# Optimization experiments

Measured on AMD Instinct MI355X. Metric: run time of the kernel, lower is better.

## Reference

```python
import jax, jax.numpy as jnp
import numpy as np

SEQ, BATCH, IN, HID, OUT = 512, 4096, 9, 64, 10


def setup_inputs() -> dict:
    key = jax.random.key(0)
    ks = jax.random.split(key, 11)
    s = 1.0 / np.sqrt(HID)
    u = lambda k, shp: jax.random.uniform(k, shp, jnp.float32, -s, s)
    return {
        "x": jax.random.normal(ks[0], (SEQ, BATCH, IN), jnp.float32),
        "W_ih0": u(ks[1], (HID, IN)),
        "W_hh0": u(ks[2], (HID, HID)),
        "b_ih0": u(ks[3], (HID,)),
        "b_hh0": u(ks[4], (HID,)),
        "W_ih1": u(ks[5], (HID, HID)),
        "W_hh1": u(ks[6], (HID, HID)),
        "b_ih1": u(ks[7], (HID,)),
        "b_hh1": u(ks[8], (HID,)),
        "W_fc": u(ks[9], (OUT, HID)),
        "b_fc": u(ks[10], (OUT,)),
    }


def _rnn_layer(x, W_ih, W_hh, b_ih, b_hh):
    # x: (seq, batch, d_in) -> (seq, batch, hid); h_t = tanh(x_t W_ih^T + b_ih + h_{t-1} W_hh^T + b_hh)
    xw = jnp.einsum('sbi,hi->sbh', x, W_ih) + (b_ih + b_hh)  # precompute input proj
    h0 = jnp.zeros((x.shape[1], W_hh.shape[0]), x.dtype)

    def step(h, xw_t):
        h = jnp.tanh(xw_t + h @ W_hh.T)
        return h, h

    _, out = jax.lax.scan(step, h0, xw)
    return out


def reference(x, W_ih0, W_hh0, b_ih0, b_hh0, W_ih1, W_hh1, b_ih1, b_hh1, W_fc, b_fc):
    h1 = _rnn_layer(x, W_ih0, W_hh0, b_ih0, b_hh0)   # (seq, batch, hid)
    h2 = _rnn_layer(h1, W_ih1, W_hh1, b_ih1, b_hh1)  # (seq, batch, hid)
    # Faithful to original quirk: rnn_out[:, -1, :] on a (seq, batch, hid) tensor
    # selects the last BATCH element for every timestep -> (seq, hid)
    feat = h2[:, -1, :]
    return feat @ W_fc.T + b_fc  # (seq, out)
```

## Files before the change

### kernel.cpp

```cpp
#include <hip/hip_runtime.h>

#define SEQn   512
#define BATCHn 4096
#define INn    9
#define HIDn   64
#define OUTn   10

typedef __attribute__((ext_vector_type(4))) float f32x4;
typedef _Float16 half2_t __attribute__((ext_vector_type(2)));
typedef unsigned short u16;
typedef unsigned int   u32;

#if __has_builtin(__builtin_amdgcn_fdot2)
#define DOT2(a,b,c) __builtin_amdgcn_fdot2((a),(b),(c),false)
#else
__device__ __forceinline__ float DOT2(half2_t a, half2_t b, float c){
    return __builtin_fmaf((float)a.x,(float)b.x, __builtin_fmaf((float)a.y,(float)b.y,c));
}
#endif
#define H2(u) __builtin_bit_cast(half2_t, (u))

__device__ __forceinline__ float fast_tanh(float x){
    float e = __builtin_amdgcn_exp2f(x * 2.8853900817779268f);
    float r = __builtin_amdgcn_rcpf(e + 1.0f);
    return __builtin_fmaf(-2.0f, r, 1.0f);
}
__device__ __forceinline__ u16 f2h(float v){
    return __builtin_bit_cast(u16, (_Float16)v);
}

__device__ __forceinline__ void load_w16(const float* __restrict__ W, int row, half2_t* wr){
#pragma unroll
    for (int c = 0; c < 16; ++c){
        f32x4 v = *(const f32x4*)&W[row*HIDn + c*4];
        wr[2*c]   = half2_t{(_Float16)v.x, (_Float16)v.y};
        wr[2*c+1] = half2_t{(_Float16)v.z, (_Float16)v.w};
    }
}

__device__ __forceinline__ float dot64r(const uint4* v, const half2_t* wr, float acc){
    float a0 = acc, a1 = 0.f, a2 = 0.f, a3 = 0.f;
#pragma unroll
    for (int jb = 0; jb < 8; ++jb){
        a0 = DOT2(H2(v[jb].x), wr[jb*4+0], a0);
        a1 = DOT2(H2(v[jb].y), wr[jb*4+1], a1);
        a2 = DOT2(H2(v[jb].z), wr[jb*4+2], a2);
        a3 = DOT2(H2(v[jb].w), wr[jb*4+3], a3);
    }
    return (a0 + a1) + (a2 + a3);
}

extern "C" __global__ __launch_bounds__(256, 1)
void rnn_lastrow(const float* __restrict__ x,
                 const float* __restrict__ Wih0, const float* __restrict__ Whh0,
                 const float* __restrict__ bih0, const float* __restrict__ bhh0,
                 const float* __restrict__ Wih1, const float* __restrict__ Whh1,
                 const float* __restrict__ bih1, const float* __restrict__ bhh1,
                 const float* __restrict__ Wfc,  const float* __restrict__ bfc,
                 float* __restrict__ out)
{
    __shared__ __align__(16) u16   xl16[SEQn*16];
    __shared__ __align__(16) float u2r[64*HIDn];
    __shared__ __align__(16) u16   h1buf[HIDn];
    __shared__ __align__(16) u16   h2buf[HIDn];
    __shared__ u32 wm[2];

    const int tid  = threadIdx.x;
    const int w    = tid >> 6;
    const int lane = tid & 63;
    volatile u32* vwm = wm;

    for (int idx = tid; idx < SEQn*16; idx += 256){
        int t = idx >> 4, j = idx & 15;
        float v = (j < INn) ? x[((long)t*BATCHn + (BATCHn-1))*INn + j] : 0.f;
        xl16[idx] = f2h(v);
    }
    if (tid < 64){ h1buf[tid] = 0; h2buf[tid] = 0; }
    if (tid == 0){ wm[0] = 0u; wm[1] = 0u; }
    __syncthreads();
    if (w >= 2) return;

    if (w == 0){
        half2_t wr0[32], wr1[32], wx[5];
        load_w16(Whh0, lane, wr0);
        load_w16(Wih1, lane, wr1);
        const float* wxr = Wih0 + lane*INn;
#pragma unroll
        for (int p = 0; p < 4; ++p)
            wx[p] = half2_t{(_Float16)wxr[2*p], (_Float16)wxr[2*p+1]};
        wx[4] = half2_t{(_Float16)wxr[8], (_Float16)0.f};
        const float b1 = bih0[lane] + bhh0[lane];
        const float b2 = bih1[lane] + bhh1[lane];

        uint4 va[8], vb[8];

        auto w0step = [&](int p, uint4* CUR, const uint4* PRV){
            if ((p & 7) == 0){
                asm volatile("s_waitcnt lgkmcnt(0)" ::: "memory");
                vwm[0] = (p >= 2) ? (u32)(p - 2) : 0u;
                while (vwm[1] + 58u <= (u32)p) __builtin_amdgcn_s_sleep(2);
            }
#pragma unroll
            for (int j = 0; j < 8; ++j) CUR[j] = ((const uint4*)h1buf)[j];
            const u32* xr = (const u32*)(xl16 + p*16);
            uint4 xa = *(const uint4*)xr;
            u32  xb = xr[4];
            if (p >= 2){
                float u2v = dot64r(PRV, wr1, b2);
                u2r[((p-2)&63)*HIDn + lane] = u2v;
            }
            float u1 = b1;
            u1 = DOT2(H2(xa.x), wx[0], u1);
            u1 = DOT2(H2(xa.y), wx[1], u1);
            u1 = DOT2(H2(xa.z), wx[2], u1);
            u1 = DOT2(H2(xa.w), wx[3], u1);
            u1 = DOT2(H2(xb),   wx[4], u1);
            float y = dot64r(CUR, wr0, 0.f);
            h1buf[lane] = f2h(fast_tanh(y + u1));
        };

        for (int p = 0; p < SEQn; p += 2){
            w0step(p,     va, vb);
            w0step(p + 1, vb, va);
        }
        {
            float u2v = dot64r(vb, wr1, b2);
            u2r[(510 & 63)*HIDn + lane] = u2v;
            uint4 vf[8];
#pragma unroll
            for (int j = 0; j < 8; ++j) vf[j] = ((const uint4*)h1buf)[j];
            u2v = dot64r(vf, wr1, b2);
            u2r[(511 & 63)*HIDn + lane] = u2v;
            asm volatile("s_waitcnt lgkmcnt(0)" ::: "memory");
            vwm[0] = (u32)SEQn;
        }
    } else {
        half2_t wr2[32], wfc[32];
        load_w16(Whh1, lane, wr2);
        load_w16(Wfc, (lane < OUTn) ? lane : (OUTn-1), wfc);
        const float bo = (lane < OUTn) ? bfc[lane] : 0.f;

        uint4 va[8], vb[8];

        auto w1step = [&](int c, uint4* CUR, const uint4* PRV){
            if ((c & 7) == 0){
                vwm[1] = (u32)c;
                while (vwm[0] < (u32)(c + 8)) __builtin_amdgcn_s_sleep(2);
            }
#pragma unroll
            for (int j = 0; j < 8; ++j) CUR[j] = ((const uint4*)h2buf)[j];
            float u2v = *((volatile float*)&u2r[(c & 63)*HIDn + lane]);
            if (c >= 2 && lane < OUTn){
                float fc = dot64r(PRV, wfc, bo);
                out[(c-2)*OUTn + lane] = fc;
            }
            float y = dot64r(CUR, wr2, u2v);
            h2buf[lane] = f2h(fast_tanh(y));
        };

        for (int c = 0; c < SEQn; c += 2){
            w1step(c,     va, vb);
            w1step(c + 1, vb, va);
        }
        if (lane < OUTn){
            float fc = dot64r(vb, wfc, bo);
            out[510*OUTn + lane] = fc;
        }
        {
            uint4 vf[8];
#pragma unroll
            for (int j = 0; j < 8; ++j) vf[j] = ((const uint4*)h2buf)[j];
            if (lane < OUTn){
                float fc = dot64r(vf, wfc, bo);
                out[511*OUTn + lane] = fc;
            }
        }
    }
}

extern "C" void kernel_launch(void* const* d_in, const int* in_sizes, int n_in,
                              void* d_out, int out_size, void* d_ws, size_t ws_size,
                              hipStream_t stream){
    rnn_lastrow<<<dim3(1), dim3(256), 0, stream>>>(
        (const float*)d_in[0],
        (const float*)d_in[1], (const float*)d_in[2],
        (const float*)d_in[3], (const float*)d_in[4],
        (const float*)d_in[5], (const float*)d_in[6],
        (const float*)d_in[7], (const float*)d_in[8],
        (const float*)d_in[9], (const float*)d_in[10],
        (float*)d_out);
}
```

Before: 270.8 us.

## Replace per-lane fdot2 recurrence with MFMA 16x16x16 matvecs kept in registers

Result: slower. 394.2 us (+45.6%).

```diff
diff --git a/kernel.cpp b/kernel.cpp
--- a/kernel.cpp
+++ b/kernel.cpp
@@ -6,48 +6,22 @@
 #define HIDn   64
 #define OUTn   10
 
-typedef __attribute__((ext_vector_type(4))) float f32x4;
-typedef _Float16 half2_t __attribute__((ext_vector_type(2)));
+typedef __attribute__((ext_vector_type(4))) float    f32x4;
+typedef __attribute__((ext_vector_type(4))) _Float16 f16x4;
 typedef unsigned short u16;
 typedef unsigned int   u32;
 
-#if __has_builtin(__builtin_amdgcn_fdot2)
-#define DOT2(a,b,c) __builtin_amdgcn_fdot2((a),(b),(c),false)
-#else
-__device__ __forceinline__ float DOT2(half2_t a, half2_t b, float c){
-    return __builtin_fmaf((float)a.x,(float)b.x, __builtin_fmaf((float)a.y,(float)b.y,c));
-}
-#endif
-#define H2(u) __builtin_bit_cast(half2_t, (u))
-
-__device__ __forceinline__ float fast_tanh(float x){
-    float e = __builtin_amdgcn_exp2f(x * 2.8853900817779268f);
+#define MFMA16(A,B,C) __builtin_amdgcn_mfma_f32_16x16x16f16((A),(B),(C),0,0,0)
+
+__device__ __forceinline__ float tanh_pre(float x){
+    float e = __builtin_amdgcn_exp2f(x);
     float r = __builtin_amdgcn_rcpf(e + 1.0f);
     return __builtin_fmaf(-2.0f, r, 1.0f);
 }
-__device__ __forceinline__ u16 f2h(float v){
-    return __builtin_bit_cast(u16, (_Float16)v);
-}
-
-__device__ __forceinline__ void load_w16(const float* __restrict__ W, int row, half2_t* wr){
-#pragma unroll
-    for (int c = 0; c < 16; ++c){
-        f32x4 v = *(const f32x4*)&W[row*HIDn + c*4];
-        wr[2*c]   = half2_t{(_Float16)v.x, (_Float16)v.y};
-        wr[2*c+1] = half2_t{(_Float16)v.z, (_Float16)v.w};
-    }
-}
-
-__device__ __forceinline__ float dot64r(const uint4* v, const half2_t* wr, float acc){
-    float a0 = acc, a1 = 0.f, a2 = 0.f, a3 = 0.f;
-#pragma unroll
-    for (int jb = 0; jb < 8; ++jb){
-        a0 = DOT2(H2(v[jb].x), wr[jb*4+0], a0);
-        a1 = DOT2(H2(v[jb].y), wr[jb*4+1], a1);
-        a2 = DOT2(H2(v[jb].z), wr[jb*4+2], a2);
-        a3 = DOT2(H2(v[jb].w), wr[jb*4+3], a3);
-    }
-    return (a0 + a1) + (a2 + a3);
+__device__ __forceinline__ u16 f2h(float v){ return __builtin_bit_cast(u16, (_Float16)v); }
+__device__ __forceinline__ f16x4 cvt4(f32x4 a){
+    f16x4 r = {(_Float16)a.x, (_Float16)a.y, (_Float16)a.z, (_Float16)a.w};
+    return r;
 }
 
 extern "C" __global__ __launch_bounds__(256, 1)
@@ -61,119 +35,196 @@
 {
     __shared__ __align__(16) u16   xl16[SEQn*16];
     __shared__ __align__(16) float u2r[64*HIDn];
-    __shared__ __align__(16) u16   h1buf[HIDn];
-    __shared__ __align__(16) u16   h2buf[HIDn];
     __shared__ u32 wm[2];
 
     const int tid  = threadIdx.x;
     const int w    = tid >> 6;
     const int lane = tid & 63;
+    const int g    = lane >> 4;
+    const int n    = lane & 15;
     volatile u32* vwm = wm;
+    const float K = 2.8853900817779268f;
 
     for (int idx = tid; idx < SEQn*16; idx += 256){
         int t = idx >> 4, j = idx & 15;
         float v = (j < INn) ? x[((long)t*BATCHn + (BATCHn-1))*INn + j] : 0.f;
         xl16[idx] = f2h(v);
     }
-    if (tid < 64){ h1buf[tid] = 0; h2buf[tid] = 0; }
     if (tid == 0){ wm[0] = 0u; wm[1] = 0u; }
     __syncthreads();
     if (w >= 2) return;
 
     if (w == 0){
-        half2_t wr0[32], wr1[32], wx[5];
-        load_w16(Whh0, lane, wr0);
-        load_w16(Wih1, lane, wr1);
-        const float* wxr = Wih0 + lane*INn;
-#pragma unroll
-        for (int p = 0; p < 4; ++p)
-            wx[p] = half2_t{(_Float16)wxr[2*p], (_Float16)wxr[2*p+1]};
-        wx[4] = half2_t{(_Float16)wxr[8], (_Float16)0.f};
-        const float b1 = bih0[lane] + bhh0[lane];
-        const float b2 = bih1[lane] + bhh1[lane];
-
-        uint4 va[8], vb[8];
-
-        auto w0step = [&](int p, uint4* CUR, const uint4* PRV){
+        f16x4 wh0[4][4], wi1[4][4], wx[4];
+        f32x4 b1f[4], b2f[4];
+#pragma unroll
+        for (int r = 0; r < 4; ++r){
+            f32x4 bi  = *(const f32x4*)&bih0[16*r + 4*g];
+            f32x4 bh  = *(const f32x4*)&bhh0[16*r + 4*g];
+            b1f[r] = (bi + bh) * K;
+            f32x4 bi1 = *(const f32x4*)&bih1[16*r + 4*g];
+            f32x4 bh1 = *(const f32x4*)&bhh1[16*r + 4*g];
+            b2f[r] = (bi1 + bh1) * K;
+#pragma unroll
+            for (int c = 0; c < 4; ++c){
+                f32x4 a0 = *(const f32x4*)&Whh0[(16*r + n)*HIDn + 16*c + 4*g];
+                wh0[r][c] = cvt4(a0 * K);
+                f32x4 a1 = *(const f32x4*)&Wih1[(16*r + n)*HIDn + 16*c + 4*g];
+                wi1[r][c] = cvt4(a1 * K);
+            }
+            int base = (16*r + n)*INn, k0 = 4*g;
+            f16x4 e;
+            e.x = (_Float16)((k0+0 < INn) ? Wih0[base + k0+0]*K : 0.f);
+            e.y = (_Float16)((k0+1 < INn) ? Wih0[base + k0+1]*K : 0.f);
+            e.z = (_Float16)((k0+2 < INn) ? Wih0[base + k0+2]*K : 0.f);
+            e.w = (_Float16)((k0+3 < INn) ? Wih0[base + k0+3]*K : 0.f);
+            wx[r] = e;
+        }
+        f16x4 hz = {(_Float16)0.f, (_Float16)0.f, (_Float16)0.f, (_Float16)0.f};
+        f16x4 hb[4] = {hz, hz, hz, hz};
+
+        auto w0step = [&](int p, f16x4& XC, f16x4& XN){
             if ((p & 7) == 0){
                 asm volatile("s_waitcnt lgkmcnt(0)" ::: "memory");
-                vwm[0] = (p >= 2) ? (u32)(p - 2) : 0u;
-                while (vwm[1] + 58u <= (u32)p) __builtin_amdgcn_s_sleep(2);
-            }
-#pragma unroll
-            for (int j = 0; j < 8; ++j) CUR[j] = ((const uint4*)h1buf)[j];
-            const u32* xr = (const u32*)(xl16 + p*16);
-            uint4 xa = *(const uint4*)xr;
-            u32  xb = xr[4];
-            if (p >= 2){
-                float u2v = dot64r(PRV, wr1, b2);
-                u2r[((p-2)&63)*HIDn + lane] = u2v;
-            }
-            float u1 = b1;
-            u1 = DOT2(H2(xa.x), wx[0], u1);
-            u1 = DOT2(H2(xa.y), wx[1], u1);
-            u1 = DOT2(H2(xa.z), wx[2], u1);
-            u1 = DOT2(H2(xa.w), wx[3], u1);
-            u1 = DOT2(H2(xb),   wx[4], u1);
-            float y = dot64r(CUR, wr0, 0.f);
-            h1buf[lane] = f2h(fast_tanh(y + u1));
+                vwm[0] = (u32)(p ? p-1 : 0);
+                int guard = 1 << 20;
+                while ((vwm[1] + 56u <= (u32)p) && --guard) __builtin_amdgcn_s_sleep(2);
+                asm volatile("" ::: "memory");
+            }
+            XN = *(const f16x4*)&xl16[((p+1) & (SEQn-1))*16 + 4*g];
+            f32x4 acc[4], u2a[4];
+#pragma unroll
+            for (int r = 0; r < 4; ++r){
+                acc[r] = MFMA16(wx[r], XC, b1f[r]);
+                u2a[r] = b2f[r];
+            }
+#pragma unroll
+            for (int c = 0; c < 4; ++c)
+#pragma unroll
+                for (int r = 0; r < 4; ++r){
+                    acc[r] = MFMA16(wh0[r][c], hb[c], acc[r]);
+                    u2a[r] = MFMA16(wi1[r][c], hb[c], u2a[r]);
+                }
+            if (p && ((lane & 15) == 0)){
+                int s = (p-1) & 63;
+#pragma unroll
+                for (int r = 0; r < 4; ++r)
+                    *(f32x4*)&u2r[s*HIDn + 16*r + 4*g] = u2a[r];
+            }
+#pragma unroll
+            for (int r = 0; r < 4; ++r){
+                f32x4 t;
+                t.x = tanh_pre(acc[r].x); t.y = tanh_pre(acc[r].y);
+                t.z = tanh_pre(acc[r].z); t.w = tanh_pre(acc[r].w);
+                hb[r] = cvt4(t);
+            }
         };
 
+        f16x4 xfA = *(const f16x4*)&xl16[0*16 + 4*g];
+        f16x4 xfB;
         for (int p = 0; p < SEQn; p += 2){
-            w0step(p,     va, vb);
-            w0step(p + 1, vb, va);
+            w0step(p,     xfA, xfB);
+            w0step(p + 1, xfB, xfA);
         }
         {
-            float u2v = dot64r(vb, wr1, b2);
-            u2r[(510 & 63)*HIDn + lane] = u2v;
-            uint4 vf[8];
-#pragma unroll
-            for (int j = 0; j < 8; ++j) vf[j] = ((const uint4*)h1buf)[j];
-            u2v = dot64r(vf, wr1, b2);
-            u2r[(511 & 63)*HIDn + lane] = u2v;
+            f32x4 u2a[4];
+#pragma unroll
+            for (int r = 0; r < 4; ++r) u2a[r] = b2f[r];
+#pragma unroll
+            for (int c = 0; c < 4; ++c)
+#pragma unroll
+                for (int r = 0; r < 4; ++r)
+                    u2a[r] = MFMA16(wi1[r][c], hb[c], u2a[r]);
+            if ((lane & 15) == 0){
+                int s = (SEQn-1) & 63;
+#pragma unroll
+                for (int r = 0; r < 4; ++r)
+                    *(f32x4*)&u2r[s*HIDn + 16*r + 4*g] = u2a[r];
+            }
             asm volatile("s_waitcnt lgkmcnt(0)" ::: "memory");
-            vwm[0] = (u32)SEQn;
+            vwm[0] = 4096u;
         }
     } else {
-        half2_t wr2[32], wfc[32];
-        load_w16(Whh1, lane, wr2);
-        load_w16(Wfc, (lane < OUTn) ? lane : (OUTn-1), wfc);
-        const float bo = (lane < OUTn) ? bfc[lane] : 0.f;
-
-        uint4 va[8], vb[8];
-
-        auto w1step = [&](int c, uint4* CUR, const uint4* PRV){
+        f16x4 wh1[4][4], wfc4[4];
+        f32x4 bfcf;
+#pragma unroll
+        for (int r = 0; r < 4; ++r)
+#pragma unroll
+            for (int c = 0; c < 4; ++c){
+                f32x4 a = *(const f32x4*)&Whh1[(16*r + n)*HIDn + 16*c + 4*g];
+                wh1[r][c] = cvt4(a * K);
+            }
+        {
+            int mrow = (n < OUTn) ? n : (OUTn-1);
+#pragma unroll
+            for (int c = 0; c < 4; ++c)
+                wfc4[c] = cvt4(*(const f32x4*)&Wfc[mrow*HIDn + 16*c + 4*g]);
+            int o0 = 4*g;
+            bfcf.x = (o0+0 < OUTn) ? bfc[o0+0] : 0.f;
+            bfcf.y = (o0+1 < OUTn) ? bfc[o0+1] : 0.f;
+            bfcf.z = (o0+2 < OUTn) ? bfc[o0+2] : 0.f;
+            bfcf.w = (o0+3 < OUTn) ? bfc[o0+3] : 0.f;
+        }
+        f16x4 hz = {(_Float16)0.f, (_Float16)0.f, (_Float16)0.f, (_Float16)0.f};
+        f16x4 hb2[4] = {hz, hz, hz, hz};
+
+        auto store_fc = [&](int t, f32x4 v){
+            if (((lane & 15) == 0) && g < 3){
+                float* o = out + t*OUTn + 4*g;
+                o[0] = v.x; o[1] = v.y;
+                if (g < 2){ o[2] = v.z; o[3] = v.w; }
+            }
+        };
+        auto w1step = [&](int c, f32x4* CU, f32x4* NX){
             if ((c & 7) == 0){
                 vwm[1] = (u32)c;
-                while (vwm[0] < (u32)(c + 8)) __builtin_amdgcn_s_sleep(2);
-            }
-#pragma unroll
-            for (int j = 0; j < 8; ++j) CUR[j] = ((const uint4*)h2buf)[j];
-            float u2v = *((volatile float*)&u2r[(c & 63)*HIDn + lane]);
-            if (c >= 2 && lane < OUTn){
-                float fc = dot64r(PRV, wfc, bo);
-                out[(c-2)*OUTn + lane] = fc;
-            }
-            float y = dot64r(CUR, wr2, u2v);
-            h2buf[lane] = f2h(fast_tanh(y));
+                int guard = 1 << 20;
+                while ((vwm[0] < (u32)(c + 9)) && --guard) __builtin_amdgcn_s_sleep(2);
+                asm volatile("" ::: "memory");
+                if (c == 0){
+#pragma unroll
+                    for (int r = 0; r < 4; ++r)
+                        CU[r] = *(const f32x4*)&u2r[16*r + 4*g];
+                }
+            }
+#pragma unroll
+            for (int r = 0; r < 4; ++r)
+                NX[r] = *(const f32x4*)&u2r[((c+1) & 63)*HIDn + 16*r + 4*g];
+            if (c){
+                f32x4 fca = bfcf;
+#pragma unroll
+                for (int cc = 0; cc < 4; ++cc)
+                    fca = MFMA16(wfc4[cc], hb2[cc], fca);
+                store_fc(c-1, fca);
+            }
+            f32x4 acc[4];
+#pragma unroll
+            for (int r = 0; r < 4; ++r) acc[r] = CU[r];
+#pragma unroll
+            for (int cc = 0; cc < 4; ++cc)
+#pragma unroll
+                for (int r = 0; r < 4; ++r)
+                    acc[r] = MFMA16(wh1[r][cc], hb2[cc], acc[r]);
+#pragma unroll
+            for (int r = 0; r < 4; ++r){
+                f32x4 t;
+                t.x = tanh_pre(acc[r].x); t.y = tanh_pre(acc[r].y);
+                t.z = tanh_pre(acc[r].z); t.w = tanh_pre(acc[r].w);
+                hb2[r] = cvt4(t);
+            }
         };
 
+        f32x4 uA[4], uB[4];
         for (int c = 0; c < SEQn; c += 2){
-            w1step(c,     va, vb);
-            w1step(c + 1, vb, va);
-        }
-        if (lane < OUTn){
-            float fc = dot64r(vb, wfc, bo);
-            out[510*OUTn + lane] = fc;
+            w1step(c,     uA, uB);
+            w1step(c + 1, uB, uA);
         }
         {
-            uint4 vf[8];
-#pragma unroll
-            for (int j = 0; j < 8; ++j) vf[j] = ((const uint4*)h2buf)[j];
-            if (lane < OUTn){
-                float fc = dot64r(vf, wfc, bo);
-                out[511*OUTn + lane] = fc;
-            }
+            f32x4 fca = bfcf;
+#pragma unroll
+            for (int cc = 0; cc < 4; ++cc)
+                fca = MFMA16(wfc4[cc], hb2[cc], fca);
+            store_fc(SEQn-1, fca);
         }
     }
 }
```

## Batch off-critical-path projections into 16-step MFMA blocks using hidden-state rings

Applied to the files above, without the earlier changes.

New measurement: 241.1 us. 11.0% less time.

```diff
diff --git a/kernel.cpp b/kernel.cpp
--- a/kernel.cpp
+++ b/kernel.cpp
@@ -5,11 +5,16 @@
 #define INn    9
 #define HIDn   64
 #define OUTn   10
-
-typedef __attribute__((ext_vector_type(4))) float f32x4;
+#define ROW1   72
+#define U2P    72
+
+typedef __attribute__((ext_vector_type(4))) float    f32x4;
+typedef __attribute__((ext_vector_type(4))) _Float16 f16x4;
 typedef _Float16 half2_t __attribute__((ext_vector_type(2)));
 typedef unsigned short u16;
 typedef unsigned int   u32;
+
+#define MFMA16(A,B,C) __builtin_amdgcn_mfma_f32_16x16x16f16((A),(B),(C),0,0,0)
 
 #if __has_builtin(__builtin_amdgcn_fdot2)
 #define DOT2(a,b,c) __builtin_amdgcn_fdot2((a),(b),(c),false)
@@ -20,21 +25,23 @@
 #endif
 #define H2(u) __builtin_bit_cast(half2_t, (u))
 
-__device__ __forceinline__ float fast_tanh(float x){
-    float e = __builtin_amdgcn_exp2f(x * 2.8853900817779268f);
+__device__ __forceinline__ float tanh_pre(float x){
+    float e = __builtin_amdgcn_exp2f(x);
     float r = __builtin_amdgcn_rcpf(e + 1.0f);
     return __builtin_fmaf(-2.0f, r, 1.0f);
 }
-__device__ __forceinline__ u16 f2h(float v){
-    return __builtin_bit_cast(u16, (_Float16)v);
-}
-
-__device__ __forceinline__ void load_w16(const float* __restrict__ W, int row, half2_t* wr){
+__device__ __forceinline__ u16 f2h(float v){ return __builtin_bit_cast(u16, (_Float16)v); }
+__device__ __forceinline__ f16x4 cvt4(f32x4 a){
+    f16x4 r = {(_Float16)a.x, (_Float16)a.y, (_Float16)a.z, (_Float16)a.w};
+    return r;
+}
+
+__device__ __forceinline__ void load_w16s(const float* __restrict__ W, int row, float s, half2_t* wr){
 #pragma unroll
     for (int c = 0; c < 16; ++c){
         f32x4 v = *(const f32x4*)&W[row*HIDn + c*4];
-        wr[2*c]   = half2_t{(_Float16)v.x, (_Float16)v.y};
-        wr[2*c+1] = half2_t{(_Float16)v.z, (_Float16)v.w};
+        wr[2*c]   = half2_t{(_Float16)(v.x*s), (_Float16)(v.y*s)};
+        wr[2*c+1] = half2_t{(_Float16)(v.z*s), (_Float16)(v.w*s)};
     }
 }
 
@@ -60,121 +67,154 @@
                  float* __restrict__ out)
 {
     __shared__ __align__(16) u16   xl16[SEQn*16];
-    __shared__ __align__(16) float u2r[64*HIDn];
-    __shared__ __align__(16) u16   h1buf[HIDn];
-    __shared__ __align__(16) u16   h2buf[HIDn];
+    __shared__ __align__(16) float u2r[64*U2P];
+    __shared__ __align__(16) u16   ring1[16*ROW1];
+    __shared__ __align__(16) u16   ring2[16*ROW1];
     __shared__ u32 wm[2];
 
     const int tid  = threadIdx.x;
     const int w    = tid >> 6;
     const int lane = tid & 63;
+    const int g    = lane >> 4;
+    const int n    = lane & 15;
     volatile u32* vwm = wm;
+    const float K = 2.8853900817779268f;
 
     for (int idx = tid; idx < SEQn*16; idx += 256){
         int t = idx >> 4, j = idx & 15;
         float v = (j < INn) ? x[((long)t*BATCHn + (BATCHn-1))*INn + j] : 0.f;
         xl16[idx] = f2h(v);
     }
-    if (tid < 64){ h1buf[tid] = 0; h2buf[tid] = 0; }
+    for (int idx = tid; idx < 16*ROW1; idx += 256){ ring1[idx] = 0; ring2[idx] = 0; }
     if (tid == 0){ wm[0] = 0u; wm[1] = 0u; }
     __syncthreads();
     if (w >= 2) return;
 
     if (w == 0){
-        half2_t wr0[32], wr1[32], wx[5];
-        load_w16(Whh0, lane, wr0);
-        load_w16(Wih1, lane, wr1);
-        const float* wxr = Wih0 + lane*INn;
-#pragma unroll
-        for (int p = 0; p < 4; ++p)
-            wx[p] = half2_t{(_Float16)wxr[2*p], (_Float16)wxr[2*p+1]};
-        wx[4] = half2_t{(_Float16)wxr[8], (_Float16)0.f};
-        const float b1 = bih0[lane] + bhh0[lane];
-        const float b2 = bih1[lane] + bhh1[lane];
-
-        uint4 va[8], vb[8];
-
-        auto w0step = [&](int p, uint4* CUR, const uint4* PRV){
-            if ((p & 7) == 0){
+        half2_t wr0[32], wx[5];
+        load_w16s(Whh0, lane, K, wr0);
+        {
+            const float* wxr = Wih0 + lane*INn;
+#pragma unroll
+            for (int q = 0; q < 4; ++q)
+                wx[q] = half2_t{(_Float16)(wxr[2*q]*K), (_Float16)(wxr[2*q+1]*K)};
+            wx[4] = half2_t{(_Float16)(wxr[8]*K), (_Float16)0.f};
+        }
+        const float b1 = (bih0[lane] + bhh0[lane]) * K;
+
+        f16x4 wi1[4][4]; f32x4 b2f[4];
+#pragma unroll
+        for (int r = 0; r < 4; ++r){
+            f32x4 bi1 = *(const f32x4*)&bih1[16*r + 4*g];
+            f32x4 bh1 = *(const f32x4*)&bhh1[16*r + 4*g];
+            b2f[r] = (bi1 + bh1) * K;
+#pragma unroll
+            for (int c = 0; c < 4; ++c){
+                f32x4 a1 = *(const f32x4*)&Wih1[(16*r + n)*HIDn + 16*c + 4*g];
+                wi1[r][c] = cvt4(a1 * K);
+            }
+        }
+
+        auto u2batch = [&](int p0){
+            f16x4 B[4];
+#pragma unroll
+            for (int c = 0; c < 4; ++c)
+                B[c] = *(const f16x4*)&ring1[n*ROW1 + 16*c + 4*g];
+            f32x4 D[4];
+#pragma unroll
+            for (int r = 0; r < 4; ++r) D[r] = b2f[r];
+#pragma unroll
+            for (int c = 0; c < 4; ++c)
+#pragma unroll
+                for (int r = 0; r < 4; ++r)
+                    D[r] = MFMA16(wi1[r][c], B[c], D[r]);
+            int t = (p0 - 16 + n) & 63;
+#pragma unroll
+            for (int r = 0; r < 4; ++r)
+                *(f32x4*)&u2r[t*U2P + 16*r + 4*g] = D[r];
+        };
+
+        for (int p = 0; p < SEQn; ++p){
+            if ((p & 15) == 0 && p){
+                int guard = 1 << 20;
+                while ((vwm[1] + 64u <= (u32)p) && --guard) __builtin_amdgcn_s_sleep(2);
+                asm volatile("" ::: "memory");
+                u2batch(p);
                 asm volatile("s_waitcnt lgkmcnt(0)" ::: "memory");
-                vwm[0] = (p >= 2) ? (u32)(p - 2) : 0u;
-                while (vwm[1] + 58u <= (u32)p) __builtin_amdgcn_s_sleep(2);
+                vwm[0] = (u32)p;
             }
-#pragma unroll
-            for (int j = 0; j < 8; ++j) CUR[j] = ((const uint4*)h1buf)[j];
             const u32* xr = (const u32*)(xl16 + p*16);
             uint4 xa = *(const uint4*)xr;
-            u32  xb = xr[4];
-            if (p >= 2){
-                float u2v = dot64r(PRV, wr1, b2);
-                u2r[((p-2)&63)*HIDn + lane] = u2v;
-            }
+            u32  xb  = xr[4];
+            uint4 CUR[8];
+            const uint4* hrow = (const uint4*)(ring1 + ((p-1) & 15)*ROW1);
+#pragma unroll
+            for (int j = 0; j < 8; ++j) CUR[j] = hrow[j];
             float u1 = b1;
             u1 = DOT2(H2(xa.x), wx[0], u1);
             u1 = DOT2(H2(xa.y), wx[1], u1);
             u1 = DOT2(H2(xa.z), wx[2], u1);
             u1 = DOT2(H2(xa.w), wx[3], u1);
             u1 = DOT2(H2(xb),   wx[4], u1);
-            float y = dot64r(CUR, wr0, 0.f);
-            h1buf[lane] = f2h(fast_tanh(y + u1));
-        };
-
-        for (int p = 0; p < SEQn; p += 2){
-            w0step(p,     va, vb);
-            w0step(p + 1, vb, va);
+            float y = dot64r(CUR, wr0, u1);
+            ring1[(p & 15)*ROW1 + lane] = f2h(tanh_pre(y));
         }
         {
-            float u2v = dot64r(vb, wr1, b2);
-            u2r[(510 & 63)*HIDn + lane] = u2v;
-            uint4 vf[8];
-#pragma unroll
-            for (int j = 0; j < 8; ++j) vf[j] = ((const uint4*)h1buf)[j];
-            u2v = dot64r(vf, wr1, b2);
-            u2r[(511 & 63)*HIDn + lane] = u2v;
+            int guard = 1 << 20;
+            while ((vwm[1] + 64u <= (u32)SEQn) && --guard) __builtin_amdgcn_s_sleep(2);
+            asm volatile("" ::: "memory");
+            u2batch(SEQn);
             asm volatile("s_waitcnt lgkmcnt(0)" ::: "memory");
             vwm[0] = (u32)SEQn;
         }
     } else {
-        half2_t wr2[32], wfc[32];
-        load_w16(Whh1, lane, wr2);
-        load_w16(Wfc, (lane < OUTn) ? lane : (OUTn-1), wfc);
-        const float bo = (lane < OUTn) ? bfc[lane] : 0.f;
-
-        uint4 va[8], vb[8];
-
-        auto w1step = [&](int c, uint4* CUR, const uint4* PRV){
-            if ((c & 7) == 0){
+        half2_t wr2[32];
+        load_w16s(Whh1, lane, K, wr2);
+        f16x4 wfcA[4]; f32x4 bfcf;
+        {
+            int mrow = (n < OUTn) ? n : (OUTn - 1);
+#pragma unroll
+            for (int c = 0; c < 4; ++c)
+                wfcA[c] = cvt4(*(const f32x4*)&Wfc[mrow*HIDn + 16*c + 4*g]);
+            int o0 = 4*g;
+            bfcf.x = (o0+0 < OUTn) ? bfc[o0+0] : 0.f;
+            bfcf.y = (o0+1 < OUTn) ? bfc[o0+1] : 0.f;
+            bfcf.z = (o0+2 < OUTn) ? bfc[o0+2] : 0.f;
+            bfcf.w = (o0+3 < OUTn) ? bfc[o0+3] : 0.f;
+        }
+
+        auto fcbatch = [&](int c0){
+            f16x4 B[4];
+#pragma unroll
+            for (int c = 0; c < 4; ++c)
+                B[c] = *(const f16x4*)&ring2[n*ROW1 + 16*c + 4*g];
+            f32x4 D = bfcf;
+#pragma unroll
+            for (int c = 0; c < 4; ++c)
+                D = MFMA16(wfcA[c], B[c], D);
+            int t = c0 - 16 + n;
+            float* o = out + t*OUTn + 4*g;
+            if (g < 2){ o[0] = D.x; o[1] = D.y; o[2] = D.z; o[3] = D.w; }
+            else if (g == 2){ o[0] = D.x; o[1] = D.y; }
+        };
+
+        for (int c = 0; c < SEQn; ++c){
+            if ((c & 15) == 0){
                 vwm[1] = (u32)c;
-                while (vwm[0] < (u32)(c + 8)) __builtin_amdgcn_s_sleep(2);
+                if (c) fcbatch(c);
+                int guard = 1 << 20;
+                while ((vwm[0] < (u32)(c + 16)) && --guard) __builtin_amdgcn_s_sleep(1);
+                asm volatile("" ::: "memory");
             }
-#pragma unroll
-            for (int j = 0; j < 8; ++j) CUR[j] = ((const uint4*)h2buf)[j];
-            float u2v = *((volatile float*)&u2r[(c & 63)*HIDn + lane]);
-            if (c >= 2 && lane < OUTn){
-                float fc = dot64r(PRV, wfc, bo);
-                out[(c-2)*OUTn + lane] = fc;
-            }
+            float u2v = u2r[(c & 63)*U2P + lane];
+            uint4 CUR[8];
+            const uint4* hrow = (const uint4*)(ring2 + ((c-1) & 15)*ROW1);
+#pragma unroll
+            for (int j = 0; j < 8; ++j) CUR[j] = hrow[j];
             float y = dot64r(CUR, wr2, u2v);
-            h2buf[lane] = f2h(fast_tanh(y));
-        };
-
-        for (int c = 0; c < SEQn; c += 2){
-            w1step(c,     va, vb);
-            w1step(c + 1, vb, va);
-        }
-        if (lane < OUTn){
-            float fc = dot64r(vb, wfc, bo);
-            out[510*OUTn + lane] = fc;
-        }
-        {
-            uint4 vf[8];
-#pragma unroll
-            for (int j = 0; j < 8; ++j) vf[j] = ((const uint4*)h2buf)[j];
-            if (lane < OUTn){
-                float fc = dot64r(vf, wfc, bo);
-                out[511*OUTn + lane] = fc;
-            }
-        }
+            ring2[(c & 15)*ROW1 + lane] = f2h(tanh_pre(y));
+        }
+        fcbatch(SEQn);
     }
 }
 
```
